# Kernel optimization log

Hardware: AMD Instinct MI355X
Metric: run time of the kernel (lower is better)

The kernel has to match this reference:

```python
import jax, jax.numpy as jnp
import numpy as np
from jax import lax

KS = 3          # kernel size
PAD = 1         # zero padding
N = KS * KS     # sampling points per output pixel


def _deform_conv(x, w_off, b_off, w_conv):
    """Deformable conv (4uiiurz1-style): offsets from a 3x3 conv, bilinear
    sampling of KS*KS points per pixel, then a 1-pixel KSxKS contraction.
    x: [B,C,H,W]; w_off: [2N,C,3,3]; b_off: [2N]; w_conv: [O,C,3,3]."""
    B, C, H, W = x.shape
    # offset field: [B, 2N, H, W]
    offset = lax.conv_general_dilated(
        x, w_off, window_strides=(1, 1), padding=((PAD, PAD), (PAD, PAD)),
        dimension_numbers=("NCHW", "OIHW", "NCHW")) + b_off[None, :, None, None]
    off = jnp.transpose(offset, (0, 2, 3, 1))  # [B,H,W,2N]

    xp = jnp.pad(x, ((0, 0), (0, 0), (PAD, PAD), (PAD, PAD)))
    Hp, Wp = H + 2 * PAD, W + 2 * PAD

    # sampling positions in padded coords: p = p0 + p_n + offset
    rng = jnp.arange(-(KS - 1) // 2, (KS - 1) // 2 + 1, dtype=x.dtype)
    pn_x, pn_y = jnp.meshgrid(rng, rng, indexing="ij")  # row-major: n = i*KS + j
    p0_x = jnp.arange(1, H + 1, dtype=x.dtype)
    p0_y = jnp.arange(1, W + 1, dtype=x.dtype)
    px = off[..., :N] + p0_x[None, :, None, None] + pn_x.ravel()  # [B,H,W,N]
    py = off[..., N:] + p0_y[None, None, :, None] + pn_y.ravel()

    fx = jnp.floor(px)
    fy = jnp.floor(py)
    qlt_x = jnp.clip(fx, 0, Hp - 1)
    qlt_y = jnp.clip(fy, 0, Wp - 1)
    qrb_x = jnp.clip(fx + 1, 0, Hp - 1)
    qrb_y = jnp.clip(fy + 1, 0, Wp - 1)
    pxc = jnp.clip(px, 0, Hp - 1)
    pyc = jnp.clip(py, 0, Wp - 1)

    # bilinear weights (exact form of the torch reference)
    g_lt = (1 + (qlt_x - pxc)) * (1 + (qlt_y - pyc))
    g_rb = (1 - (qrb_x - pxc)) * (1 - (qrb_y - pyc))
    g_lb = (1 + (qlt_x - pxc)) * (1 - (qrb_y - pyc))
    g_rt = (1 - (qrb_x - pxc)) * (1 + (qlt_y - pyc))

    xf = xp.reshape(B, C, Hp * Wp)

    def gather(qx, qy):
        idx = (qx.astype(jnp.int32) * Wp + qy.astype(jnp.int32)).reshape(B, 1, -1)
        return jnp.take_along_axis(xf, idx, axis=2).reshape(B, C, H, W, N)

    x_lt = gather(qlt_x, qlt_y)
    x_rb = gather(qrb_x, qrb_y)
    x_lb = gather(qlt_x, qrb_y)
    x_rt = gather(qrb_x, qlt_y)

    x_off = (g_lt[:, None] * x_lt + g_rb[:, None] * x_rb +
             g_lb[:, None] * x_lb + g_rt[:, None] * x_rt)  # [B,C,H,W,N]

    # equivalent of tiling to [B,C,H*KS,W*KS] then conv(k=KS, s=KS), no bias
    O = w_conv.shape[0]
    return jnp.einsum("bchwn,ocn->bohw", x_off, w_conv.reshape(O, C, N))


def setup_inputs() -> dict:
    key = jax.random.key(0)
    ks = jax.random.split(key, 7)
    B, C, H, W = 2, 64, 256, 256
    x = jax.random.normal(ks[0], (B, C, H, W), dtype=jnp.float32)
    w_off1 = jax.random.normal(ks[1], (2 * N, C, KS, KS), dtype=jnp.float32) * 0.01
    b_off1 = jax.random.normal(ks[2], (2 * N,), dtype=jnp.float32) * 0.01
    w1 = jax.random.normal(ks[3], (C, C, KS, KS), dtype=jnp.float32) * (1.0 / np.sqrt(C * N))
    w_off2 = jax.random.normal(ks[4], (2 * N, C, KS, KS), dtype=jnp.float32) * 0.01
    b_off2 = jax.random.normal(ks[5], (2 * N,), dtype=jnp.float32) * 0.01
    w2 = jax.random.normal(ks[6], (C, C, KS, KS), dtype=jnp.float32) * (1.0 / np.sqrt(C * N))
    return {"x": x, "w_off1": w_off1, "b_off1": b_off1, "w1": w1,
            "w_off2": w_off2, "b_off2": b_off2, "w2": w2}


def reference(x, w_off1, b_off1, w1, w_off2, b_off2, w2):
    res = _deform_conv(x, w_off1, b_off1, w1)
    res = jax.nn.relu(res)
    res = _deform_conv(res, w_off2, b_off2, w2)
    return x + res
```

## Files before the change

kernel.cpp:

```cpp
#include <hip/hip_runtime.h>


typedef __attribute__((ext_vector_type(8))) short short8;
typedef __attribute__((ext_vector_type(4))) float float4a;
typedef __attribute__((ext_vector_type(2))) float f32x2;

static __device__ __forceinline__ unsigned int cvtpk(float lo, float hi) {
    unsigned int r;
    asm("v_cvt_pk_bf16_f32 %0, %1, %2" : "=v"(r) : "v"(lo), "v"(hi));
    return r;
}
static __device__ __forceinline__ unsigned short f2bf(float f) {
    return (unsigned short)(cvtpk(f, f) & 0xffffu);
}
static __device__ __forceinline__ float bflo(unsigned int u) {
    return __builtin_bit_cast(float, u << 16);
}
static __device__ __forceinline__ float bfhi(unsigned int u) {
    return __builtin_bit_cast(float, u & 0xffff0000u);
}
static __device__ __forceinline__ f32x2 up2(unsigned int u) {
    f32x2 r; r.x = bflo(u); r.y = bfhi(u); return r;
}
static __device__ __forceinline__ unsigned int comb2(unsigned int A, unsigned int B,
                                                     unsigned int C, unsigned int D,
                                                     f32x2 gx, f32x2 gy,
                                                     f32x2 gz, f32x2 gw) {
    f32x2 acc = gx * up2(A) + gy * up2(B) + gz * up2(C) + gw * up2(D);
    return cvtpk(acc.x, acc.y);
}
static __device__ __forceinline__ uint4 comb16(const uint4 V0, const uint4 V1,
                                               const uint4 V2, const uint4 V3,
                                               float4 g) {
    f32x2 gx; gx.x = g.x; gx.y = g.x;
    f32x2 gy; gy.x = g.y; gy.y = g.y;
    f32x2 gz; gz.x = g.z; gz.y = g.z;
    f32x2 gw; gw.x = g.w; gw.y = g.w;
    uint4 r;
    r.x = comb2(V0.x, V1.x, V2.x, V3.x, gx, gy, gz, gw);
    r.y = comb2(V0.y, V1.y, V2.y, V3.y, gx, gy, gz, gw);
    r.z = comb2(V0.z, V1.z, V2.z, V3.z, gx, gy, gz, gw);
    r.w = comb2(V0.w, V1.w, V2.w, V3.w, gx, gy, gz, gw);
    return r;
}
static __device__ __forceinline__ void decode_rec(const uint2 r, int4& li, float4& gg) {
    const unsigned int base = r.x & 0xFFFFu;
    const unsigned int m = r.x >> 16;
    const float dx = (float)__builtin_bit_cast(_Float16, (unsigned short)(r.y & 0xFFFFu));
    const float dy = (float)__builtin_bit_cast(_Float16, (unsigned short)(r.y >> 16));
    const float omx = 1.f - dx, omy = 1.f - dy;
    li.x = (m & 1u) ? (int)base : 0;
    li.y = (m & 2u) ? (int)((base + 257u) & 0xFFFFu) : 0;
    li.z = (m & 4u) ? (int)((base + 1u) & 0xFFFFu) : 0;
    li.w = (m & 8u) ? (int)((base + 256u) & 0xFFFFu) : 0;
    gg.x = (m & 1u) ? omx * omy : 0.f;
    gg.y = (m & 2u) ? dx * dy : 0.f;
    gg.z = (m & 4u) ? omx * dy : 0.f;
    gg.w = (m & 8u) ? dx * omy : 0.f;
}

__global__ __launch_bounds__(256) void k_pack_all(const float* __restrict__ w1,
                                                  const float* __restrict__ w2,
                                                  const float* __restrict__ wo1,
                                                  const float* __restrict__ wo2,
                                                  unsigned short* __restrict__ w1b,
                                                  unsigned short* __restrict__ w2b,
                                                  unsigned short* __restrict__ wob1,
                                                  unsigned short* __restrict__ wob2) {
    int i = blockIdx.x * 256 + threadIdx.x;
    if (i < 36864) {
        int o = i / 576, k = i - o * 576, n = k >> 6, c = k & 63;
        int dst = (((o >> 4) * 18 + (k >> 5)) * 64 + (((k >> 3) & 3) << 4) + (o & 15)) * 8 + (k & 7);
        w1b[dst] = f2bf(w1[o * 576 + c * 9 + n]);
    } else if (i < 73728) {
        int j = i - 36864;
        int o = j / 576, k = j - o * 576, n = k >> 6, c = k & 63;
        int dst = (((o >> 4) * 18 + (k >> 5)) * 64 + (((k >> 3) & 3) << 4) + (o & 15)) * 8 + (k & 7);
        w2b[dst] = f2bf(w2[o * 576 + c * 9 + n]);
    } else if (i < 92160) {
        int j = i - 73728;
        int oc = j / 576, k = j - oc * 576, n = k >> 6, c = k & 63;
        int dst = (((oc >> 4) * 18 + (k >> 5)) * 64 + (((k >> 3) & 3) << 4) + (oc & 15)) * 8 + (k & 7);
        wob1[dst] = (oc < 18) ? f2bf(wo1[oc * 576 + c * 9 + n]) : (unsigned short)0;
    } else if (i < 110592) {
        int j = i - 92160;
        int oc = j / 576, k = j - oc * 576, n = k >> 6, c = k & 63;
        int dst = (((oc >> 4) * 18 + (k >> 5)) * 64 + (((k >> 3) & 3) << 4) + (oc & 15)) * 8 + (k & 7);
        wob2[dst] = (oc < 18) ? f2bf(wo2[oc * 576 + c * 9 + n]) : (unsigned short)0;
    }
}

__global__ __launch_bounds__(256) void k_transpose_bf(const float* __restrict__ x,
                                                      unsigned short* __restrict__ xt) {
    __shared__ float tile[64][65];
    const float* xb = x + (size_t)blockIdx.y * 4194304;
    unsigned short* xtb = xt + (size_t)blockIdx.y * 4194304;
    const int p0 = blockIdx.x << 6;
    const int p = threadIdx.x & 63;
    const int c0 = threadIdx.x >> 6;
    #pragma unroll
    for (int i = 0; i < 16; ++i) {
        const int c = (i << 2) + c0;
        tile[p][c] = xb[(c << 16) + p0 + p];
    }
    __syncthreads();
    const int cq = (threadIdx.x & 15) << 2;
    const int pr0 = threadIdx.x >> 4;
    #pragma unroll
    for (int j = 0; j < 4; ++j) {
        const int pr = (j << 4) + pr0;
        uint2 u;
        u.x = cvtpk(tile[pr][cq + 0], tile[pr][cq + 1]);
        u.y = cvtpk(tile[pr][cq + 2], tile[pr][cq + 3]);
        *(uint2*)(xtb + ((p0 + pr) << 6) + cq) = u;
    }
}

#define GW 66

__global__ __launch_bounds__(256) void k_geom(const unsigned short* __restrict__ src,
                                              const unsigned short* __restrict__ wob,
                                              const float* __restrict__ b_off,
                                              uint2* __restrict__ tbl,
                                              int row_base, int Rrows) {
    __shared__ unsigned short s_win[4 * GW * 64];
    __shared__ float          s_soff[4 * 320];

    const int b = blockIdx.z;
    const int h0 = row_base + (blockIdx.y << 1);
    const int tid = threadIdx.x;
    const int lane = tid & 63;
    const int wv = tid >> 6;
    const int l16 = lane & 15;
    const int q = lane >> 4;
    const int wb = blockIdx.x << 6;
    const int w0 = wb + (wv << 4);
    const unsigned short* srcb = src + ((size_t)b << 22);

    #pragma unroll
    for (int it = 0; it < 9; ++it) {
        const int i = it * 256 + tid;
        if (i < 2112) {
            const int o = i & 7;
            const int t = i >> 3;
            const int r = t / GW;
            const int cl = t - r * GW;
            const int row = h0 - 1 + r;
            const int col = wb - 1 + cl;
            const bool inb = (row >= 0) && (row < 256) && (col >= 0) && (col < 256);
            const int lin = inb ? ((row << 8) + col) : 0;
            uint4 v = *(const uint4*)(srcb + (lin << 6) + (o << 3));
            if (!inb) { v.x = 0u; v.y = 0u; v.z = 0u; v.w = 0u; }
            *(uint4*)(s_win + ((r * GW + cl) << 6) + ((o ^ (cl & 7)) << 3)) = v;
        }
    }
    __syncthreads();

    const unsigned short* bo0 = wob + lane * 8;
    const unsigned short* bo1 = wob + 9216 + lane * 8;
    float* soff = s_soff + wv * 320;

    for (int rr = 0; rr < 2; ++rr) {
        const int h = h0 + rr;

        float4a aO0 = {0.f, 0.f, 0.f, 0.f};
        float4a aO1 = {0.f, 0.f, 0.f, 0.f};
        #pragma unroll
        for (int n = 0; n < 9; ++n) {
            const int rn = n / 3, cn = n - rn * 3;
            const int cl = (wv << 4) + l16 + cn;
            const int sw = cl & 7;
            const unsigned short* cell = s_win + (((rn + rr) * GW + cl) << 6);
            const short8 a0 = *(const short8*)(cell + ((q ^ sw) << 3));
            const short8 a1 = *(const short8*)(cell + (((q + 4) ^ sw) << 3));
            const short8 wf0a = *(const short8*)(bo0 + (2 * n) * 512);
            const short8 wf0b = *(const short8*)(bo0 + (2 * n + 1) * 512);
            const short8 wf1a = *(const short8*)(bo1 + (2 * n) * 512);
            const short8 wf1b = *(const short8*)(bo1 + (2 * n + 1) * 512);
            aO0 = __builtin_amdgcn_mfma_f32_16x16x32_bf16(a0, wf0a, aO0, 0, 0, 0);
            aO0 = __builtin_amdgcn_mfma_f32_16x16x32_bf16(a1, wf0b, aO0, 0, 0, 0);
            aO1 = __builtin_amdgcn_mfma_f32_16x16x32_bf16(a0, wf1a, aO1, 0, 0, 0);
            aO1 = __builtin_amdgcn_mfma_f32_16x16x32_bf16(a1, wf1b, aO1, 0, 0, 0);
        }
        {
            const float bia0 = b_off[l16];
            #pragma unroll
            for (int r = 0; r < 4; ++r)
                soff[(q * 4 + r) * 20 + l16] = aO0[r] + bia0;
            if (l16 < 2) {
                const float bia1 = b_off[16 + l16];
                #pragma unroll
                for (int r = 0; r < 4; ++r)
                    soff[(q * 4 + r) * 20 + 16 + l16] = aO1[r] + bia1;
            }
        }

        uint2* trow = tbl + ((((size_t)(b * Rrows + (h - row_base)) << 8) + w0) * 9);
        #pragma unroll
        for (int i = 0; i < 3; ++i) {
            const int idx = i * 64 + lane;
            if (idx < 144) {
                const int px = idx / 9;
                const int n = idx - px * 9;
                const float ox = soff[px * 20 + n];
                const float oy = soff[px * 20 + 9 + n];
                const float pxx = ox + (float)(h + (n / 3));
                const float pyy = oy + (float)(w0 + px + (n % 3));
                const float fx = floorf(pxx), fy = floorf(pyy);
                const float qltx = fminf(fmaxf(fx, 0.f), 257.f);
                const float qlty = fminf(fmaxf(fy, 0.f), 257.f);
                const float qrbx = fminf(fmaxf(fx + 1.f, 0.f), 257.f);
                const float qrby = fminf(fmaxf(fy + 1.f, 0.f), 257.f);
                const int ilx = (int)qltx, ily = (int)qlty;
                const int irx = (int)qrbx, iry = (int)qrby;
                const unsigned int b0 = (ilx >= 1) && (ilx <= 256) && (ily >= 1) && (ily <= 256);
                const unsigned int b1 = (irx >= 1) && (irx <= 256) && (iry >= 1) && (iry <= 256);
                const unsigned int b2 = (ilx >= 1) && (ilx <= 256) && (iry >= 1) && (iry <= 256);
                const unsigned int b3 = (irx >= 1) && (irx <= 256) && (ily >= 1) && (ily <= 256);
                const float dx = pxx - fx;
                const float dy = pyy - fy;
                const unsigned int base =
                    ((unsigned int)(((ilx - 1) << 8) + (ily - 1))) & 0xFFFFu;
                const unsigned int m = b0 | (b1 << 1) | (b2 << 2) | (b3 << 3);
                const unsigned int hx = __builtin_bit_cast(unsigned short, (_Float16)dx);
                const unsigned int hy = __builtin_bit_cast(unsigned short, (_Float16)dy);
                uint2 rec;
                rec.x = base | (m << 16);
                rec.y = hx | (hy << 16);
                trow[px * 9 + n] = rec;
            }
        }
    }
}

#define XSTR 584

template<int TN>
static __device__ __forceinline__ void gather_round(const unsigned short* __restrict__ srcb,
                                                    int oct, const int4* L, const float4* G,
                                                    const int* nT, int t0,
                                                    unsigned short* __restrict__ s_dst) {
    uint4 V[TN][4];
    #pragma unroll
    for (int t = 0; t < TN; ++t) {
        V[t][0] = *(const uint4*)(srcb + (L[t0 + t].x << 6) + (oct << 3));
        V[t][1] = *(const uint4*)(srcb + (L[t0 + t].y << 6) + (oct << 3));
        V[t][2] = *(const uint4*)(srcb + (L[t0 + t].z << 6) + (oct << 3));
        V[t][3] = *(const uint4*)(srcb + (L[t0 + t].w << 6) + (oct << 3));
    }
    #pragma unroll
    for (int t = 0; t < TN; ++t) {
        const uint4 r = comb16(V[t][0], V[t][1], V[t][2], V[t][3], G[t0 + t]);
        *(uint4*)(s_dst + (nT[t0 + t] << 6) + (oct << 3)) = r;
    }
}

static __device__ __forceinline__ void epilogue_seg(float4a acc, int b, int h, int segw,
                                                    int wave, int quad, int l16,
                                                    int relu, int nhwc_out,
                                                    const float* __restrict__ addsrc,
                                                    void* __restrict__ out) {
    const int o = wave * 16 + l16;
    if (nhwc_out) {
        unsigned short* ob = (unsigned short*)out + ((size_t)b << 22);
        unsigned short* orow = ob + ((((h << 8) + segw) << 6)) + o;
        #pragma unroll
        for (int r = 0; r < 4; ++r) {
            float v = acc[r];
            if (relu) v = fmaxf(v, 0.f);
            orow[(size_t)((quad * 4 + r) << 6)] = f2bf(v);
        }
    } else {
        float* obf = (float*)out + ((size_t)b << 22);
        const int gidx = (o << 16) + (h << 8) + segw + (quad << 2);
        float v0 = acc[0], v1 = acc[1], v2 = acc[2], v3 = acc[3];
        if (relu) {
            v0 = fmaxf(v0, 0.f); v1 = fmaxf(v1, 0.f);
            v2 = fmaxf(v2, 0.f); v3 = fmaxf(v3, 0.f);
        }
        if (addsrc != nullptr) {
            const float4 rv = *(const float4*)(addsrc + ((size_t)b << 22) + gidx);
            v0 += rv.x; v1 += rv.y; v2 += rv.z; v3 += rv.w;
        }
        float4 vv; vv.x = v0; vv.y = v1; vv.z = v2; vv.w = v3;
        *(float4*)(obf + gidx) = vv;
    }
}

__global__ __launch_bounds__(256, 3) void k_gconv(const unsigned short* __restrict__ src,
                                                  const uint2* __restrict__ tbl,
                                                  const unsigned short* __restrict__ wtb,
                                                  const float* __restrict__ addsrc,
                                                  void* __restrict__ out,
                                                  int relu, int nhwc_out,
                                                  int row_base, int Rrows) {
    __shared__ unsigned short s_xoff[16 * XSTR];

    const int b = blockIdx.z;
    const int h = row_base + blockIdx.y;
    const int w0 = blockIdx.x << 5;
    const int tid = threadIdx.x;
    const int lane = tid & 63;
    const int wave = tid >> 6;
    const int quad = lane >> 4;
    const int l16 = lane & 15;

    const int px = tid >> 4;
    const int oct = tid & 7;
    const int g = (tid >> 3) & 1;
    const unsigned short* srcb = src + ((size_t)b << 22);

    const int nT[5] = {g ? 1 : 0, g ? 3 : 2, g ? 5 : 4, g ? 7 : 6, g ? 7 : 8};

    const uint2* trow = tbl + ((((size_t)(b * Rrows + blockIdx.y) << 8) + w0) * 9);
    uint2 R0[5], R1[5];
    #pragma unroll
    for (int t = 0; t < 5; ++t) R0[t] = trow[px * 9 + nT[t]];
    #pragma unroll
    for (int t = 0; t < 5; ++t) R1[t] = trow[(16 + px) * 9 + nT[t]];

    int4 L0[5]; float4 G0[5];
    #pragma unroll
    for (int t = 0; t < 5; ++t) decode_rec(R0[t], L0[t], G0[t]);

    unsigned short* s_dst = s_xoff + px * XSTR;

    gather_round<3>(srcb, oct, L0, G0, nT, 0, s_dst);
    gather_round<2>(srcb, oct, L0, G0, nT, 3, s_dst);

    int4 L1[5]; float4 G1[5];
    #pragma unroll
    for (int t = 0; t < 5; ++t) decode_rec(R1[t], L1[t], G1[t]);
    uint4 E[3][4];
    #pragma unroll
    for (int t = 0; t < 3; ++t) {
        E[t][0] = *(const uint4*)(srcb + (L1[t].x << 6) + (oct << 3));
        E[t][1] = *(const uint4*)(srcb + (L1[t].y << 6) + (oct << 3));
        E[t][2] = *(const uint4*)(srcb + (L1[t].z << 6) + (oct << 3));
        E[t][3] = *(const uint4*)(srcb + (L1[t].w << 6) + (oct << 3));
    }
    __builtin_amdgcn_sched_barrier(0);
    __syncthreads();

    const unsigned short* bw = wtb + wave * 9216 + lane * 8;
    const unsigned short* arow = s_xoff + l16 * XSTR + quad * 8;
    float4a acc0 = {0.f, 0.f, 0.f, 0.f};
    #pragma unroll
    for (int ks = 0; ks < 18; ++ks) {
        const short8 a = *(const short8*)(arow + ks * 32);
        const short8 bf = *(const short8*)(bw + ks * 512);
        acc0 = __builtin_amdgcn_mfma_f32_16x16x32_bf16(a, bf, acc0, 0, 0, 0);
    }
    epilogue_seg(acc0, b, h, w0, wave, quad, l16, relu, nhwc_out, addsrc, out);

    __syncthreads();

    uint4 F[2][4];
    #pragma unroll
    for (int t = 0; t < 2; ++t) {
        F[t][0] = *(const uint4*)(srcb + (L1[3 + t].x << 6) + (oct << 3));
        F[t][1] = *(const uint4*)(srcb + (L1[3 + t].y << 6) + (oct << 3));
        F[t][2] = *(const uint4*)(srcb + (L1[3 + t].z << 6) + (oct << 3));
        F[t][3] = *(const uint4*)(srcb + (L1[3 + t].w << 6) + (oct << 3));
    }
    #pragma unroll
    for (int t = 0; t < 3; ++t) {
        const uint4 r = comb16(E[t][0], E[t][1], E[t][2], E[t][3], G1[t]);
        *(uint4*)(s_dst + (nT[t] << 6) + (oct << 3)) = r;
    }
    #pragma unroll
    for (int t = 0; t < 2; ++t) {
        const uint4 r = comb16(F[t][0], F[t][1], F[t][2], F[t][3], G1[3 + t]);
        *(uint4*)(s_dst + (nT[3 + t] << 6) + (oct << 3)) = r;
    }
    __syncthreads();

    float4a acc1 = {0.f, 0.f, 0.f, 0.f};
    #pragma unroll
    for (int ks = 0; ks < 18; ++ks) {
        const short8 a = *(const short8*)(arow + ks * 32);
        const short8 bf = *(const short8*)(bw + ks * 512);
        acc1 = __builtin_amdgcn_mfma_f32_16x16x32_bf16(a, bf, acc1, 0, 0, 0);
    }
    epilogue_seg(acc1, b, h, w0 + 16, wave, quad, l16, relu, nhwc_out, addsrc, out);
}

extern "C" void kernel_launch(void* const* d_in, const int* in_sizes, int n_in,
                              void* d_out, int out_size, void* d_ws, size_t ws_size,
                              hipStream_t stream) {
    const float* x      = (const float*)d_in[0];
    const float* w_off1 = (const float*)d_in[1];
    const float* b_off1 = (const float*)d_in[2];
    const float* w1     = (const float*)d_in[3];
    const float* w_off2 = (const float*)d_in[4];
    const float* b_off2 = (const float*)d_in[5];
    const float* w2     = (const float*)d_in[6];
    float* outp = (float*)d_out;

    char* ws = (char*)d_ws;
    unsigned short* xT   = (unsigned short*)ws;
    unsigned short* midT = (unsigned short*)(ws + 16777216);
    unsigned short* w1b  = (unsigned short*)(ws + 33554432);
    unsigned short* w2b  = (unsigned short*)(ws + 33554432 + 73728);
    unsigned short* wob1 = (unsigned short*)(ws + 33554432 + 2 * 73728);
    unsigned short* wob2 = (unsigned short*)(ws + 33554432 + 2 * 73728 + 36864);
    const size_t fixed = 33554432 + 2 * 73728 + 2 * 36864;
    uint2* tbl = (uint2*)(ws + fixed);

    int R = 256;
    if (ws_size != 0) {
        size_t avail = (ws_size > fixed) ? (ws_size - fixed) : 0;
        while (R > 32 && (size_t)R * 36864ull > avail) R >>= 1;
    }

    k_pack_all<<<432, 256, 0, stream>>>(w1, w2, w_off1, w_off2, w1b, w2b, wob1, wob2);

    dim3 gT(1024, 2);
    k_transpose_bf<<<gT, 256, 0, stream>>>(x, xT);

    for (int r0 = 0; r0 < 256; r0 += R) {
        dim3 gG(4, R >> 1, 2), gC(8, R, 2);
        k_geom<<<gG, 256, 0, stream>>>(xT, wob1, b_off1, tbl, r0, R);
        k_gconv<<<gC, 256, 0, stream>>>(xT, tbl, w1b, nullptr, midT, 1, 1, r0, R);
    }
    for (int r0 = 0; r0 < 256; r0 += R) {
        dim3 gG(4, R >> 1, 2), gC(8, R, 2);
        k_geom<<<gG, 256, 0, stream>>>(midT, wob2, b_off2, tbl, r0, R);
        k_gconv<<<gC, 256, 0, stream>>>(midT, tbl, w2b, x, outp, 0, 0, r0, R);
    }
}
```

Measured before the change: 234.6 us.

## Process four 16-pixel segments per gconv block with software-pipelined gathers

Each k_gconv block now covers 64 output pixels instead of 32, looping over four 16-pixel segments. The gather loads for the next segment are issued before the current segment's MFMA and epilogue run, and the table records for the segment after that are prefetched, so global-load latency overlaps the matrix work. This halves the grid size and amortizes block setup across more work. In exchange it adds extra barriers per block and keeps more live registers, and the smaller grid leaves less parallelism to hide latency.

```diff
diff --git a/kernel.cpp b/kernel.cpp
--- a/kernel.cpp
+++ b/kernel.cpp
@@ -255,6 +255,41 @@
     }
 }
 
+static __device__ __forceinline__ void issue3(const unsigned short* __restrict__ srcb,
+                                              int oct, const int4* L, uint4 E[3][4]) {
+    #pragma unroll
+    for (int t = 0; t < 3; ++t) {
+        E[t][0] = *(const uint4*)(srcb + (L[t].x << 6) + (oct << 3));
+        E[t][1] = *(const uint4*)(srcb + (L[t].y << 6) + (oct << 3));
+        E[t][2] = *(const uint4*)(srcb + (L[t].z << 6) + (oct << 3));
+        E[t][3] = *(const uint4*)(srcb + (L[t].w << 6) + (oct << 3));
+    }
+}
+static __device__ __forceinline__ void issue2(const unsigned short* __restrict__ srcb,
+                                              int oct, const int4* L, uint4 F[2][4]) {
+    #pragma unroll
+    for (int t = 0; t < 2; ++t) {
+        F[t][0] = *(const uint4*)(srcb + (L[3 + t].x << 6) + (oct << 3));
+        F[t][1] = *(const uint4*)(srcb + (L[3 + t].y << 6) + (oct << 3));
+        F[t][2] = *(const uint4*)(srcb + (L[3 + t].z << 6) + (oct << 3));
+        F[t][3] = *(const uint4*)(srcb + (L[3 + t].w << 6) + (oct << 3));
+    }
+}
+static __device__ __forceinline__ void comb_store(uint4 E[3][4], uint4 F[2][4],
+                                                  const float4* G, const int* nT,
+                                                  int oct, unsigned short* __restrict__ s_dst) {
+    #pragma unroll
+    for (int t = 0; t < 3; ++t) {
+        const uint4 r = comb16(E[t][0], E[t][1], E[t][2], E[t][3], G[t]);
+        *(uint4*)(s_dst + (nT[t] << 6) + (oct << 3)) = r;
+    }
+    #pragma unroll
+    for (int t = 0; t < 2; ++t) {
+        const uint4 r = comb16(F[t][0], F[t][1], F[t][2], F[t][3], G[3 + t]);
+        *(uint4*)(s_dst + (nT[3 + t] << 6) + (oct << 3)) = r;
+    }
+}
+
 static __device__ __forceinline__ void epilogue_seg(float4a acc, int b, int h, int segw,
                                                     int wave, int quad, int l16,
                                                     int relu, int nhwc_out,
@@ -287,6 +322,23 @@
     }
 }
 
+static __device__ __forceinline__ void mfma_epi(const unsigned short* __restrict__ arow,
+                                                const unsigned short* __restrict__ bw,
+                                                int b, int h, int segw,
+                                                int wave, int quad, int l16,
+                                                int relu, int nhwc_out,
+                                                const float* __restrict__ addsrc,
+                                                void* __restrict__ out) {
+    float4a acc = {0.f, 0.f, 0.f, 0.f};
+    #pragma unroll
+    for (int ks = 0; ks < 18; ++ks) {
+        const short8 a = *(const short8*)(arow + ks * 32);
+        const short8 bf = *(const short8*)(bw + ks * 512);
+        acc = __builtin_amdgcn_mfma_f32_16x16x32_bf16(a, bf, acc, 0, 0, 0);
+    }
+    epilogue_seg(acc, b, h, segw, wave, quad, l16, relu, nhwc_out, addsrc, out);
+}
+
 __global__ __launch_bounds__(256, 3) void k_gconv(const unsigned short* __restrict__ src,
                                                   const uint2* __restrict__ tbl,
                                                   const unsigned short* __restrict__ wtb,
@@ -298,7 +350,7 @@
 
     const int b = blockIdx.z;
     const int h = row_base + blockIdx.y;
-    const int w0 = blockIdx.x << 5;
+    const int w0 = blockIdx.x << 6;
     const int tid = threadIdx.x;
     const int lane = tid & 63;
     const int wave = tid >> 6;
@@ -313,76 +365,70 @@
     const int nT[5] = {g ? 1 : 0, g ? 3 : 2, g ? 5 : 4, g ? 7 : 6, g ? 7 : 8};
 
     const uint2* trow = tbl + ((((size_t)(b * Rrows + blockIdx.y) << 8) + w0) * 9);
-    uint2 R0[5], R1[5];
-    #pragma unroll
-    for (int t = 0; t < 5; ++t) R0[t] = trow[px * 9 + nT[t]];
-    #pragma unroll
-    for (int t = 0; t < 5; ++t) R1[t] = trow[(16 + px) * 9 + nT[t]];
-
-    int4 L0[5]; float4 G0[5];
-    #pragma unroll
-    for (int t = 0; t < 5; ++t) decode_rec(R0[t], L0[t], G0[t]);
-
-    unsigned short* s_dst = s_xoff + px * XSTR;
-
-    gather_round<3>(srcb, oct, L0, G0, nT, 0, s_dst);
-    gather_round<2>(srcb, oct, L0, G0, nT, 3, s_dst);
-
-    int4 L1[5]; float4 G1[5];
-    #pragma unroll
-    for (int t = 0; t < 5; ++t) decode_rec(R1[t], L1[t], G1[t]);
-    uint4 E[3][4];
-    #pragma unroll
-    for (int t = 0; t < 3; ++t) {
-        E[t][0] = *(const uint4*)(srcb + (L1[t].x << 6) + (oct << 3));
-        E[t][1] = *(const uint4*)(srcb + (L1[t].y << 6) + (oct << 3));
-        E[t][2] = *(const uint4*)(srcb + (L1[t].z << 6) + (oct << 3));
-        E[t][3] = *(const uint4*)(srcb + (L1[t].w << 6) + (oct << 3));
-    }
-    __builtin_amdgcn_sched_barrier(0);
-    __syncthreads();
-
     const unsigned short* bw = wtb + wave * 9216 + lane * 8;
     const unsigned short* arow = s_xoff + l16 * XSTR + quad * 8;
-    float4a acc0 = {0.f, 0.f, 0.f, 0.f};
-    #pragma unroll
-    for (int ks = 0; ks < 18; ++ks) {
-        const short8 a = *(const short8*)(arow + ks * 32);
-        const short8 bf = *(const short8*)(bw + ks * 512);
-        acc0 = __builtin_amdgcn_mfma_f32_16x16x32_bf16(a, bf, acc0, 0, 0, 0);
-    }
-    epilogue_seg(acc0, b, h, w0, wave, quad, l16, relu, nhwc_out, addsrc, out);
-
-    __syncthreads();
-
+    unsigned short* s_dst = s_xoff + px * XSTR;
+
+    uint2 Ra[5], Rb[5];
+    #pragma unroll
+    for (int t = 0; t < 5; ++t) Ra[t] = trow[px * 9 + nT[t]];
+    #pragma unroll
+    for (int t = 0; t < 5; ++t) Rb[t] = trow[(16 + px) * 9 + nT[t]];
+
+    int4 L[5]; float4 G[5];
+    #pragma unroll
+    for (int t = 0; t < 5; ++t) decode_rec(Ra[t], L[t], G[t]);
+
+    gather_round<3>(srcb, oct, L, G, nT, 0, s_dst);
+    gather_round<2>(srcb, oct, L, G, nT, 3, s_dst);
+
+    #pragma unroll
+    for (int t = 0; t < 5; ++t) decode_rec(Rb[t], L[t], G[t]);
+    uint4 E[3][4];
+    issue3(srcb, oct, L, E);
+    __builtin_amdgcn_sched_barrier(0);
+    __syncthreads();
+
+    #pragma unroll
+    for (int t = 0; t < 5; ++t) Ra[t] = trow[(32 + px) * 9 + nT[t]];
+
+    mfma_epi(arow, bw, b, h, w0, wave, quad, l16, relu, nhwc_out, addsrc, out);
     uint4 F[2][4];
-    #pragma unroll
-    for (int t = 0; t < 2; ++t) {
-        F[t][0] = *(const uint4*)(srcb + (L1[3 + t].x << 6) + (oct << 3));
-        F[t][1] = *(const uint4*)(srcb + (L1[3 + t].y << 6) + (oct << 3));
-        F[t][2] = *(const uint4*)(srcb + (L1[3 + t].z << 6) + (oct << 3));
-        F[t][3] = *(const uint4*)(srcb + (L1[3 + t].w << 6) + (oct << 3));
-    }
-    #pragma unroll
-    for (int t = 0; t < 3; ++t) {
-        const uint4 r = comb16(E[t][0], E[t][1], E[t][2], E[t][3], G1[t]);
-        *(uint4*)(s_dst + (nT[t] << 6) + (oct << 3)) = r;
-    }
-    #pragma unroll
-    for (int t = 0; t < 2; ++t) {
-        const uint4 r = comb16(F[t][0], F[t][1], F[t][2], F[t][3], G1[3 + t]);
-        *(uint4*)(s_dst + (nT[3 + t] << 6) + (oct << 3)) = r;
-    }
-    __syncthreads();
-
-    float4a acc1 = {0.f, 0.f, 0.f, 0.f};
-    #pragma unroll
-    for (int ks = 0; ks < 18; ++ks) {
-        const short8 a = *(const short8*)(arow + ks * 32);
-        const short8 bf = *(const short8*)(bw + ks * 512);
-        acc1 = __builtin_amdgcn_mfma_f32_16x16x32_bf16(a, bf, acc1, 0, 0, 0);
-    }
-    epilogue_seg(acc1, b, h, w0 + 16, wave, quad, l16, relu, nhwc_out, addsrc, out);
+    issue2(srcb, oct, L, F);
+    __builtin_amdgcn_sched_barrier(0);
+    __syncthreads();
+
+    comb_store(E, F, G, nT, oct, s_dst);
+    #pragma unroll
+    for (int t = 0; t < 5; ++t) decode_rec(Ra[t], L[t], G[t]);
+    issue3(srcb, oct, L, E);
+    __builtin_amdgcn_sched_barrier(0);
+    __syncthreads();
+
+    #pragma unroll
+    for (int t = 0; t < 5; ++t) Rb[t] = trow[(48 + px) * 9 + nT[t]];
+
+    mfma_epi(arow, bw, b, h, w0 + 16, wave, quad, l16, relu, nhwc_out, addsrc, out);
+    issue2(srcb, oct, L, F);
+    __builtin_amdgcn_sched_barrier(0);
+    __syncthreads();
+
+    comb_store(E, F, G, nT, oct, s_dst);
+    #pragma unroll
+    for (int t = 0; t < 5; ++t) decode_rec(Rb[t], L[t], G[t]);
+    issue3(srcb, oct, L, E);
+    __builtin_amdgcn_sched_barrier(0);
+    __syncthreads();
+
+    mfma_epi(arow, bw, b, h, w0 + 32, wave, quad, l16, relu, nhwc_out, addsrc, out);
+    issue2(srcb, oct, L, F);
+    __builtin_amdgcn_sched_barrier(0);
+    __syncthreads();
+
+    comb_store(E, F, G, nT, oct, s_dst);
+    __syncthreads();
+
+    mfma_epi(arow, bw, b, h, w0 + 48, wave, quad, l16, relu, nhwc_out, addsrc, out);
 }
 
 extern "C" void kernel_launch(void* const* d_in, const int* in_sizes, int n_in,
@@ -419,12 +465,12 @@
     k_transpose_bf<<<gT, 256, 0, stream>>>(x, xT);
 
     for (int r0 = 0; r0 < 256; r0 += R) {
-        dim3 gG(4, R >> 1, 2), gC(8, R, 2);
+        dim3 gG(4, R >> 1, 2), gC(4, R, 2);
         k_geom<<<gG, 256, 0, stream>>>(xT, wob1, b_off1, tbl, r0, R);
         k_gconv<<<gC, 256, 0, stream>>>(xT, tbl, w1b, nullptr, midT, 1, 1, r0, R);
     }
     for (int r0 = 0; r0 < 256; r0 += R) {
-        dim3 gG(4, R >> 1, 2), gC(8, R, 2);
+        dim3 gG(4, R >> 1, 2), gC(4, R, 2);
         k_geom<<<gG, 256, 0, stream>>>(midT, wob2, b_off2, tbl, r0, R);
         k_gconv<<<gC, 256, 0, stream>>>(midT, tbl, w2b, x, outp, 0, 0, r0, R);
     }
```

Measured after the change: 270.1 us. 1.15x slower.
